# Optimization experiments

Hardware: AMD Instinct MI355X
Metric: run time of the kernel (lower is better)

Reference implementation:

```python
import jax, jax.numpy as jnp
import numpy as np

N_U = 50000   # num user nodes
N_I = 50000   # num item nodes
D = 64        # in_size == out_size
H = 128       # SemanticAttention hidden size (default)
E = 500000    # edges per meta-path graph
NEG_SLOPE = 0.01


def setup_inputs() -> dict:
    key = jax.random.key(0)
    ks = jax.random.split(key, 24)
    rn = lambda k, shp, s=0.1: jax.random.normal(k, shp, jnp.float32) * s
    ri = lambda k, shp, n: jax.random.randint(k, shp, 0, n, dtype=jnp.int32)
    return dict(
        feat_user=rn(ks[0], (N_U, D)), feat_item=rn(ks[1], (N_I, D)),
        attn_l=rn(ks[2], (4, D)), attn_r=rn(ks[3], (4, D)),
        W_gc=rn(ks[4], (4, D, D)), b_gc=jnp.zeros((4, D), jnp.float32),
        sa_rel_W1=rn(ks[5], (D, H)), sa_rel_b1=jnp.zeros((H,), jnp.float32), sa_rel_w2=rn(ks[6], (H,)),
        sa_u_W1=rn(ks[7], (D, H)), sa_u_b1=jnp.zeros((H,), jnp.float32), sa_u_w2=rn(ks[8], (H,)),
        sa_i_W1=rn(ks[9], (D, H)), sa_i_b1=jnp.zeros((H,), jnp.float32), sa_i_w2=rn(ks[10], (H,)),
        rel_u_src=ri(ks[11], (2, E), N_I), rel_u_dst=ri(ks[12], (2, E), N_U),
        rel_i_src=ri(ks[13], (2, E), N_U), rel_i_dst=ri(ks[14], (2, E), N_I),
        mp_u_src=ri(ks[15], (2, E), N_U), mp_u_dst=ri(ks[16], (2, E), N_U),
        mp_i_src=ri(ks[17], (2, E), N_I), mp_i_dst=ri(ks[18], (2, E), N_I),
    )


def _edge_softmax(e, dst, n_dst):
    # segment-wise (per destination node) softmax over irregular edges
    m = jax.ops.segment_max(e, dst, num_segments=n_dst)
    ex = jnp.exp(e - m[dst])
    s = jax.ops.segment_sum(ex, dst, num_segments=n_dst)
    return ex / s[dst]


def _heco_gat(src, dst, feat_src, feat_dst, al, ar, n_dst):
    # HeCoGATConv: el = sum(ft_src*attn_l), er = sum(ft_dst*attn_r)
    el = feat_src @ al  # (N_src,)
    er = feat_dst @ ar  # (N_dst,)
    e = jax.nn.leaky_relu(el[src] + er[dst], NEG_SLOPE)  # (E,)
    a = _edge_softmax(e, dst, n_dst)
    out = jax.ops.segment_sum(feat_src[src] * a[:, None], dst, num_segments=n_dst)
    return jax.nn.elu(out)


def _graph_conv(src, dst, feat, W, b, n):
    # DGL GraphConv with norm='both', activation=elu
    ones = jnp.ones(src.shape, jnp.float32)
    deg_out = jax.ops.segment_sum(ones, src, num_segments=n)
    deg_in = jax.ops.segment_sum(ones, dst, num_segments=n)
    no = jnp.where(deg_out > 0, deg_out, 1.0) ** -0.5
    ni = jnp.where(deg_in > 0, deg_in, 1.0) ** -0.5
    h = feat * no[:, None]
    agg = jax.ops.segment_sum(h[src], dst, num_segments=n)
    agg = agg * ni[:, None]
    return jax.nn.elu(agg @ W + b)


def _semantic_attention(z, W1, b1, w2):
    # z: (N, M, D) -> (N, D)
    w = (jnp.tanh(z @ W1 + b1) @ w2).mean(0)  # (M,)
    beta = jax.nn.softmax(w)
    return jnp.einsum('nmd,m->nd', z, beta)


def reference(feat_user, feat_item, attn_l, attn_r, W_gc, b_gc,
              sa_rel_W1, sa_rel_b1, sa_rel_w2,
              sa_u_W1, sa_u_b1, sa_u_w2,
              sa_i_W1, sa_i_b1, sa_i_w2,
              rel_u_src, rel_u_dst, rel_i_src, rel_i_dst,
              mp_u_src, mp_u_dst, mp_i_src, mp_i_dst):
    # --- RelationalAGG: HeCo GAT over schema-level relations ---
    zu = jnp.stack([
        _heco_gat(rel_u_src[0], rel_u_dst[0], feat_item, feat_user, attn_l[0], attn_r[0], N_U),
        _heco_gat(rel_u_src[1], rel_u_dst[1], feat_item, feat_user, attn_l[1], attn_r[1], N_U),
    ], axis=1)  # (N_U, 2, D)
    rel_u = _semantic_attention(zu, sa_rel_W1, sa_rel_b1, sa_rel_w2)
    zi = jnp.stack([
        _heco_gat(rel_i_src[0], rel_i_dst[0], feat_user, feat_item, attn_l[2], attn_r[2], N_I),
        _heco_gat(rel_i_src[1], rel_i_dst[1], feat_user, feat_item, attn_l[3], attn_r[3], N_I),
    ], axis=1)
    rel_i = _semantic_attention(zi, sa_rel_W1, sa_rel_b1, sa_rel_w2)
    # --- HAN layers: GraphConv over meta-path reachable graphs ---
    hu = jnp.stack([
        _graph_conv(mp_u_src[0], mp_u_dst[0], feat_user, W_gc[0], b_gc[0], N_U),
        _graph_conv(mp_u_src[1], mp_u_dst[1], feat_user, W_gc[1], b_gc[1], N_U),
    ], axis=1)
    han_u = _semantic_attention(hu, sa_u_W1, sa_u_b1, sa_u_w2)
    hi = jnp.stack([
        _graph_conv(mp_i_src[0], mp_i_dst[0], feat_item, W_gc[2], b_gc[2], N_I),
        _graph_conv(mp_i_src[1], mp_i_dst[1], feat_item, W_gc[3], b_gc[3], N_I),
    ], axis=1)
    han_i = _semantic_attention(hi, sa_i_W1, sa_i_b1, sa_i_w2)
    user_emb = rel_u + han_u
    item_emb = rel_i + han_i
    return jnp.concatenate([user_emb, item_emb], axis=0)  # (N_U + N_I, D)
```

## Files before the change

### kernel.cpp

```cpp
#include <hip/hip_runtime.h>
#include <math.h>

#define NU 50000
#define NI 50000
#define NN 50000
#define DD 64
#define HHID 128
#define EE 500000
#define NEG_SLOPE 0.01f
#define NBKT 196
#define CAP 3072
#define TILE 8192
#define TPG 62
#define P1T 512
#define NIMG 12
#define AGGB 1563
#define SEMB 512

typedef _Float16 half_t;
typedef _Float16 half8 __attribute__((ext_vector_type(8)));
typedef _Float16 half4 __attribute__((ext_vector_type(4)));
typedef float f32x4 __attribute__((ext_vector_type(4)));
union H4 { uint2 u; half_t h[4]; };
union H8 { uint4 u; half_t h[8]; };
union HS { half8 h; int i[4]; uint4 u; };
union HS4 { half4 h; int i[2]; uint2 u; };
union HC { unsigned short us; half_t h; };

struct Ptr4c { const float* p[4]; };
struct Ptr4m { float*       p[4]; };
struct EdgeArgs { const int* src[8]; const int* dst[8]; };
struct GatArgs { const half_t* fsrc[4]; half_t* zout[4]; };
struct GcArgs  { const half_t* feat[4]; half_t* hout[4]; };
struct WArgs   { const float* el[4]; const float* er[4]; const int* deg_src; };
struct SemArgs { const half_t* z[4]; const float* W1[4]; const float* b1[4]; const float* w2[4]; };
struct PrepArgs {
    const float* featI; const float* featU;
    Ptr4c vi; Ptr4c vu; Ptr4m oi; Ptr4m ou;
    half_t* FBI; half_t* FBU;
    const float* W_gc; half_t* W16;
};

__global__ __launch_bounds__(256) void prep_kernel(PrepArgs pa) {
    int b = blockIdx.x;
    int t = threadIdx.x;
    if (b == 6250) {
        int g = t >> 6;
        int lane = t & 63;
        int cl = lane & 15, quad = lane >> 4;
#pragma unroll
        for (int nt = 0; nt < 4; nt++) {
#pragma unroll
            for (int kh = 0; kh < 2; kh++) {
                H8 o;
#pragma unroll
                for (int j = 0; j < 8; j++) {
                    int k = kh * 32 + quad * 8 + j;
                    int n = nt * 16 + cl;
                    o.h[j] = (half_t)pa.W_gc[g * 4096 + k * 64 + n];
                }
                *(uint4*)(pa.W16 + ((g * 8 + nt * 2 + kh) * 64 + lane) * 8) = o.u;
            }
        }
        return;
    }
    const float* feat; Ptr4c vecs; Ptr4m outs; half_t* fb16; int bb;
    if (b < 3125) { feat = pa.featI; vecs = pa.vi; outs = pa.oi; fb16 = pa.FBI; bb = b; }
    else          { feat = pa.featU; vecs = pa.vu; outs = pa.ou; fb16 = pa.FBU; bb = b - 3125; }
    int w = bb * 4 + (t >> 6);
    int lane = t & 63;
    int sub = lane >> 4, r = lane & 15;
    int node = w * 4 + sub;
    float4 f = *(const float4*)(feat + node * DD + r * 4);
    H4 o16;
    o16.h[0] = (half_t)f.x; o16.h[1] = (half_t)f.y; o16.h[2] = (half_t)f.z; o16.h[3] = (half_t)f.w;
    *(uint2*)(fb16 + node * DD + r * 4) = o16.u;
#pragma unroll
    for (int j = 0; j < 4; j++) {
        float4 vv = *(const float4*)(vecs.p[j] + r * 4);
        float val = f.x * vv.x + f.y * vv.y + f.z * vv.z + f.w * vv.w;
        val += __shfl_down(val, 8);
        val += __shfl_down(val, 4);
        val += __shfl_down(val, 2);
        val += __shfl_down(val, 1);
        if (r == 0) outs.p[j][node] = val;
    }
}

__global__ __launch_bounds__(P1T) void part1_kernel(EdgeArgs a, int* __restrict__ ccnt,
                                                    int* __restrict__ coarse) {
    __shared__ int bc_cnt[256], bc_scan[256], bc_start[256], bc_cur[256], bc_gbase[256];
    __shared__ int stage[TILE];
    int t = threadIdx.x;
    int g = blockIdx.x / TPG;
    int tile = blockIdx.x % TPG;
    int e0 = tile * TILE;
    int tile_n = min(TILE, EE - e0);
    bool cnt_only = g >= 8;
    const int* gk = (cnt_only ? a.src[g - 4] : a.dst[g]) + e0;
    const int* gs = cnt_only ? gk : (a.src[g] + e0);
    if (t < 256) bc_cnt[t] = 0;
    __syncthreads();
    for (int pos = t * 4; pos < tile_n; pos += P1T * 4) {
        int4 k4 = *(const int4*)(gk + pos);
        atomicAdd(&bc_cnt[k4.x >> 8], 1);
        atomicAdd(&bc_cnt[k4.y >> 8], 1);
        atomicAdd(&bc_cnt[k4.z >> 8], 1);
        atomicAdd(&bc_cnt[k4.w >> 8], 1);
    }
    __syncthreads();
    if (t < 256) bc_scan[t] = bc_cnt[t];
    __syncthreads();
    for (int off = 1; off < 256; off <<= 1) {
        int v = (t < 256 && t >= off) ? bc_scan[t - off] : 0;
        __syncthreads();
        if (t < 256) bc_scan[t] += v;
        __syncthreads();
    }
    if (t < 256) {
        int st = bc_scan[t] - bc_cnt[t];
        bc_start[t] = st;
        bc_cur[t] = st;
        bc_gbase[t] = (t < NBKT && bc_cnt[t] > 0) ? atomicAdd(&ccnt[g * NBKT + t], bc_cnt[t]) : 0;
    }
    __syncthreads();
    for (int pos = t * 4; pos < tile_n; pos += P1T * 4) {
        int4 k4 = *(const int4*)(gk + pos);
        int4 s4;
        if (cnt_only) { s4 = make_int4(0, 0, 0, 0); }
        else          { s4 = *(const int4*)(gs + pos); }
        int b0 = k4.x >> 8, b1 = k4.y >> 8, b2 = k4.z >> 8, b3 = k4.w >> 8;
        int sl0 = atomicAdd(&bc_cur[b0], 1);
        int sl1 = atomicAdd(&bc_cur[b1], 1);
        int sl2 = atomicAdd(&bc_cur[b2], 1);
        int sl3 = atomicAdd(&bc_cur[b3], 1);
        stage[sl0] = s4.x | ((k4.x & 255) << 16) | (b0 << 24);
        stage[sl1] = s4.y | ((k4.y & 255) << 16) | (b1 << 24);
        stage[sl2] = s4.z | ((k4.z & 255) << 16) | (b2 << 24);
        stage[sl3] = s4.w | ((k4.w & 255) << 16) | (b3 << 24);
    }
    __syncthreads();
    for (int j = t; j < tile_n; j += P1T) {
        int p = stage[j];
        int b = (unsigned)p >> 24;
        int pos = bc_gbase[b] + (j - bc_start[b]);
        if (pos < CAP) coarse[(g * NBKT + b) * CAP + pos] = p & 0x00FFFFFF;
    }
}

__global__ __launch_bounds__(256) void degcnt_kernel(const int* __restrict__ ccnt,
                                                     const int* __restrict__ coarse,
                                                     int* __restrict__ DEG_SRC) {
    __shared__ int cnt[256];
    int t = threadIdx.x;
    int g2 = blockIdx.x / NBKT;
    int b = blockIdx.x % NBKT;
    int img = 8 + g2;
    int n = min(ccnt[img * NBKT + b], CAP);
    cnt[t] = 0;
    __syncthreads();
    const int* pairs = coarse + (img * NBKT + b) * CAP;
    for (int i = t; i < n; i += 256) atomicAdd(&cnt[(pairs[i] >> 16) & 255], 1);
    __syncthreads();
    int v = (b << 8) + t;
    if (v < NN) DEG_SRC[g2 * NN + v] = cnt[t];
}

__global__ __launch_bounds__(256) void part2_kernel(const int* __restrict__ ccnt,
                                                    const int* __restrict__ coarse,
                                                    WArgs wa,
                                                    int* __restrict__ bucket,
                                                    int2* __restrict__ RD) {
    __shared__ int sb[256];
    __shared__ int cnt5[256], off5[256], s2[256];
    __shared__ int ordered[CAP];
    int t = threadIdx.x;
    int g = blockIdx.x / NBKT;
    int b = blockIdx.x % NBKT;
    int ccv = (t < NBKT) ? min(ccnt[g * NBKT + t], CAP) : 0;
    sb[t] = ccv;
    cnt5[t] = 0;
    __syncthreads();
    for (int off = 1; off < 256; off <<= 1) {
        int vv = (t >= off) ? sb[t - off] : 0;
        __syncthreads();
        sb[t] += vv;
        __syncthreads();
    }
    int base = (b > 0) ? sb[b - 1] : 0;
    int n = sb[b] - base;
    int node0 = b << 8;
    const int* pairs = coarse + (g * NBKT + b) * CAP;
    for (int i = t; i < n; i += 256) atomicAdd(&cnt5[pairs[i] >> 16], 1);
    __syncthreads();
    int myc = cnt5[t];
    s2[t] = myc;
    __syncthreads();
    for (int off = 1; off < 256; off <<= 1) {
        int vv = (t >= off) ? s2[t - off] : 0;
        __syncthreads();
        s2[t] += vv;
        __syncthreads();
    }
    int ex = s2[t] - myc;
    off5[t] = ex;
    int v = node0 + t;
    if (v < NN) RD[g * NN + v] = make_int2(base + ex, myc);
    __syncthreads();
    int nm1 = n - 1;
    for (int ib = t; ib < n; ib += 1024) {
        int p[4];
#pragma unroll
        for (int u = 0; u < 4; u++) {
            int i = ib + u * 256;
            p[u] = pairs[(i < n) ? i : nm1];
        }
        float w[4];
        if (g < 4) {
            float a0[4], a1[4];
#pragma unroll
            for (int u = 0; u < 4; u++) a0[u] = wa.el[g][p[u] & 0xFFFF];
#pragma unroll
            for (int u = 0; u < 4; u++) a1[u] = wa.er[g][node0 + (p[u] >> 16)];
#pragma unroll
            for (int u = 0; u < 4; u++) {
                float e = a0[u] + a1[u];
                e = (e >= 0.f) ? e : NEG_SLOPE * e;
                w[u] = __expf(e);
            }
        } else {
            int dv[4];
#pragma unroll
            for (int u = 0; u < 4; u++) dv[u] = wa.deg_src[(g - 4) * NN + (p[u] & 0xFFFF)];
#pragma unroll
            for (int u = 0; u < 4; u++) w[u] = __builtin_amdgcn_rsqf((float)dv[u]);
        }
#pragma unroll
        for (int u = 0; u < 4; u++) {
            int i = ib + u * 256;
            if (i < n) {
                HC cv; cv.h = (half_t)w[u];
                int slot = atomicAdd(&off5[p[u] >> 16], 1);
                ordered[slot] = (p[u] & 0xFFFF) | ((int)cv.us << 16);
            }
        }
    }
    __syncthreads();
    int* bko = bucket + g * EE + base;
    for (int i = t; i < n; i += 256) bko[i] = ordered[i];
}

__global__ __launch_bounds__(256) void agg_kernel(GatArgs ga, GcArgs gc, half_t* __restrict__ AGG,
                                                  const int2* __restrict__ RD,
                                                  const int* __restrict__ bucket) {
    int h = blockIdx.x / (8 * AGGB);
    int remb = blockIdx.x % (8 * AGGB);
    int g = remb / AGGB;
    int nb = remb % AGGB;
    int t = threadIdx.x;
    int wv = t >> 6, lane = t & 63;
    int q = lane >> 3, r = lane & 7;
    int v = nb * 32 + wv * 8 + q;
    bool vok = v < NN;
    int2 rd = RD[g * NN + (vok ? v : 0)];
    int start = rd.x;
    int dg = vok ? rd.y : 0;
    const int* bk = bucket + g * EE;
    const half_t* feat = (g < 4) ? ga.fsrc[g] : gc.feat[g - 4];
    int roff = h * 32 + (r << 2);
    int obase = lane & 56;
    HS4 acc[4];
#pragma unroll
    for (int a = 0; a < 4; a++) { acc[a].i[0] = 0; acc[a].i[1] = 0; }
    float s_l = 0.f;
    for (int b8 = 0; b8 < dg; b8 += 8) {
        int rem = dg - b8;
        int p = bk[start + b8 + ((r < rem) ? r : 0)];
#pragma unroll
        for (int j = 0; j < 8; j++) {
            if (j < rem) {
                int pj = __shfl(p, obase + j);
                HC wj; wj.us = (unsigned short)((unsigned)pj >> 16);
                s_l += (float)wj.h;
                HS4 row; row.u = *(const uint2*)(feat + (((pj & 0xFFFF) << 6) + roff));
                half_t wh = wj.h;
                half4 ws = {wh, wh, wh, wh};
                acc[j & 3].h += row.h * ws;
            }
        }
    }
    acc[0].h += acc[1].h;
    acc[2].h += acc[3].h;
    acc[0].h += acc[2].h;
    if (g < 4) {
        float inv = (dg > 0) ? __builtin_amdgcn_rcpf(s_l) : 0.f;
        H4 o;
#pragma unroll
        for (int i = 0; i < 4; i++) {
            float x = (float)acc[0].h[i] * inv;
            x = (x > 0.f) ? x : (__expf(x) - 1.f);
            o.h[i] = (half_t)x;
        }
        if (vok) *(uint2*)(ga.zout[g] + (v << 7) + roff) = o.u;
    } else {
        float niv = (dg > 0) ? __builtin_amdgcn_rsqf((float)dg) : 1.0f;
        H4 o;
#pragma unroll
        for (int i = 0; i < 4; i++) o.h[i] = (half_t)((float)acc[0].h[i] * niv);
        if (vok) *(uint2*)(AGG + (((g - 4) * NN + v) << 6) + roff) = o.u;
    }
}

__global__ __launch_bounds__(256) void trans_kernel(GcArgs gc, const half_t* __restrict__ AGG,
                                                    const half_t* __restrict__ W16,
                                                    const float* __restrict__ b_gc) {
    int t = threadIdx.x;
    int wv = t >> 6, lane = t & 63;
    int g = blockIdx.x / 782;
    int tile = (blockIdx.x % 782) * 4 + wv;
    if (tile >= 3125) return;
    int cl = lane & 15, quad = lane >> 4;
    const half_t* ab = AGG + ((g * NN + tile * 16 + cl) << 6);
    half8 A0 = *(const half8*)(ab + quad * 8);
    half8 A1 = *(const half8*)(ab + 32 + quad * 8);
    const half_t* wbase = W16 + g * 8 * 64 * 8;
    half_t* hout = gc.hout[g];
#pragma unroll
    for (int nt = 0; nt < 4; nt++) {
        float bb = b_gc[g * 64 + nt * 16 + cl];
        f32x4 c = {bb, bb, bb, bb};
        half8 B0 = *(const half8*)(wbase + ((nt * 2 + 0) * 64 + lane) * 8);
        half8 B1 = *(const half8*)(wbase + ((nt * 2 + 1) * 64 + lane) * 8);
        c = __builtin_amdgcn_mfma_f32_16x16x32_f16(A0, B0, c, 0, 0, 0);
        c = __builtin_amdgcn_mfma_f32_16x16x32_f16(A1, B1, c, 0, 0, 0);
#pragma unroll
        for (int r_ = 0; r_ < 4; r_++) {
            int node = tile * 16 + quad * 4 + r_;
            float x = c[r_];
            x = (x > 0.f) ? x : (__expf(x) - 1.f);
            hout[node * 128 + nt * 16 + cl] = (half_t)x;
        }
    }
}

__global__ __launch_bounds__(256) void sem_att_kernel(SemArgs sa, float* __restrict__ wsum) {
    __shared__ half_t As[2][4][1024];
    __shared__ float s0[4], s1[4];
    int inst = blockIdx.x / SEMB;
    int blk  = blockIdx.x % SEMB;
    int t = threadIdx.x;
    int wv = t >> 6, lane = t & 63;
    int quad = lane >> 4, cl = lane & 15;
    const half_t* z = sa.z[inst];
    const float* W1 = sa.W1[inst];
    half8 Bf[2][2];
    float b1v[2], w2v[2];
#pragma unroll
    for (int u = 0; u < 2; u++) {
        int nt = wv * 2 + u;
        int n = nt * 16 + cl;
#pragma unroll
        for (int kh = 0; kh < 2; kh++) {
#pragma unroll
            for (int j = 0; j < 8; j++) {
                int k = kh * 32 + quad * 8 + j;
                Bf[u][kh][j] = (half_t)W1[k * HHID + n];
            }
        }
        b1v[u] = sa.b1[inst][nt * 16 + cl];
        w2v[u] = sa.w2[inst][nt * 16 + cl];
    }
    float local0 = 0.f, local1 = 0.f;
    int K = (6250 - blk + SEMB - 1) / SEMB;
    int B = (K + 3) / 4;

#define SEM_STAGE(buf, bb) { \
    int k_ = 4 * (bb) + wv; \
    if (k_ < K) { \
        int tp_ = blk + k_ * SEMB; \
        int m_ = (tp_ >= 3125) ? 1 : 0; \
        int tm_ = tp_ - m_ * 3125; \
        int n_ = lane >> 3; \
        int j_ = (lane & 7) * 8; \
        const half_t* sA_ = z + (size_t)(tm_ * 16 + n_) * 128 + m_ * 64 + j_; \
        const half_t* sB_ = z + (size_t)(tm_ * 16 + 8 + n_) * 128 + m_ * 64 + j_; \
        __builtin_amdgcn_global_load_lds( \
            (const __attribute__((address_space(1))) unsigned int*)sA_, \
            (__attribute__((address_space(3))) unsigned int*)(&As[buf][wv][0]), 16, 0, 0); \
        __builtin_amdgcn_global_load_lds( \
            (const __attribute__((address_space(1))) unsigned int*)sB_, \
            (__attribute__((address_space(3))) unsigned int*)(&As[buf][wv][512]), 16, 0, 0); \
    } }

    int cur = 0;
    SEM_STAGE(0, 0);
    for (int b = 0; b < B; b++) {
        if (b + 1 < B) {
            SEM_STAGE(cur ^ 1, b + 1);
            asm volatile("s_waitcnt vmcnt(2)" ::: "memory");
        } else {
            asm volatile("s_waitcnt vmcnt(0)" ::: "memory");
        }
        __builtin_amdgcn_sched_barrier(0);
        __builtin_amdgcn_s_barrier();
#pragma unroll
        for (int i = 0; i < 4; i++) {
            int k = 4 * b + i;
            if (k < K) {
                int tile = blk + k * SEMB;
                const half_t* ar = &As[cur][i][cl * 64 + quad * 8];
                half8 A0 = *(const half8*)(ar);
                half8 A1 = *(const half8*)(ar + 32);
                float sumv = 0.f;
#pragma unroll
                for (int u = 0; u < 2; u++) {
                    f32x4 c = {0.f, 0.f, 0.f, 0.f};
                    c = __builtin_amdgcn_mfma_f32_16x16x32_f16(A0, Bf[u][0], c, 0, 0, 0);
                    c = __builtin_amdgcn_mfma_f32_16x16x32_f16(A1, Bf[u][1], c, 0, 0, 0);
#pragma unroll
                    for (int r = 0; r < 4; r++) {
                        float xv = c[r] + b1v[u];
                        float ev = __expf(2.f * xv);
                        float th = 1.f - 2.f * __builtin_amdgcn_rcpf(ev + 1.f);
                        sumv += th * w2v[u];
                    }
                }
                if (tile < 3125) local0 += sumv; else local1 += sumv;
            }
        }
        __builtin_amdgcn_s_barrier();
        cur ^= 1;
    }
#undef SEM_STAGE
#pragma unroll
    for (int off = 32; off > 0; off >>= 1) {
        local0 += __shfl_down(local0, off);
        local1 += __shfl_down(local1, off);
    }
    if (lane == 0) { s0[wv] = local0; s1[wv] = local1; }
    __syncthreads();
    if (t == 0) {
        float a0 = s0[0] + s0[1] + s0[2] + s0[3];
        float a1 = s1[0] + s1[1] + s1[2] + s1[3];
        if (a0 != 0.f) atomicAdd(&wsum[inst * 2 + 0], a0);
        if (a1 != 0.f) atomicAdd(&wsum[inst * 2 + 1], a1);
    }
}

__global__ void combine_kernel(const half_t* __restrict__ ZU, const half_t* __restrict__ ZI,
                               const half_t* __restrict__ HU, const half_t* __restrict__ HI,
                               const float* __restrict__ wsum, float* __restrict__ out) {
    int gid = blockIdx.x * blockDim.x + threadIdx.x;
    if (gid >= (NU + NI) * 16) return;
    int node = gid >> 4;
    int c4 = (gid & 15) * 4;
    const half_t* zb; const half_t* hb;
    float wr0, wr1, wh0, wh1;
    int idx;
    if (node < NU) {
        zb = ZU; hb = HU; idx = node;
        wr0 = wsum[0]; wr1 = wsum[1]; wh0 = wsum[4]; wh1 = wsum[5];
    } else {
        zb = ZI; hb = HI; idx = node - NU;
        wr0 = wsum[2]; wr1 = wsum[3]; wh0 = wsum[6]; wh1 = wsum[7];
    }
    const float inv_n = 1.0f / 50000.0f;
    wr0 *= inv_n; wr1 *= inv_n; wh0 *= inv_n; wh1 *= inv_n;
    float m = fmaxf(wr0, wr1);
    float e0 = __expf(wr0 - m), e1 = __expf(wr1 - m);
    float br0 = e0 / (e0 + e1), br1 = e1 / (e0 + e1);
    m = fmaxf(wh0, wh1);
    e0 = __expf(wh0 - m); e1 = __expf(wh1 - m);
    float bh0 = e0 / (e0 + e1), bh1 = e1 / (e0 + e1);
    H4 z0, z1, h0, h1;
    z0.u = *(const uint2*)(zb + idx * 128 + c4);
    z1.u = *(const uint2*)(zb + idx * 128 + 64 + c4);
    h0.u = *(const uint2*)(hb + idx * 128 + c4);
    h1.u = *(const uint2*)(hb + idx * 128 + 64 + c4);
    float4 o;
    o.x = (float)z0.h[0] * br0 + (float)z1.h[0] * br1 + (float)h0.h[0] * bh0 + (float)h1.h[0] * bh1;
    o.y = (float)z0.h[1] * br0 + (float)z1.h[1] * br1 + (float)h0.h[1] * bh0 + (float)h1.h[1] * bh1;
    o.z = (float)z0.h[2] * br0 + (float)z1.h[2] * br1 + (float)h0.h[2] * bh0 + (float)h1.h[2] * bh1;
    o.w = (float)z0.h[3] * br0 + (float)z1.h[3] * br1 + (float)h0.h[3] * bh0 + (float)h1.h[3] * bh1;
    *(float4*)(out + node * 64 + c4) = o;
}

extern "C" void kernel_launch(void* const* d_in, const int* in_sizes, int n_in,
                              void* d_out, int out_size, void* d_ws, size_t ws_size,
                              hipStream_t stream) {
    const float* feat_user = (const float*)d_in[0];
    const float* feat_item = (const float*)d_in[1];
    const float* attn_l    = (const float*)d_in[2];
    const float* attn_r    = (const float*)d_in[3];
    const float* W_gc      = (const float*)d_in[4];
    const float* b_gc      = (const float*)d_in[5];
    const float* sa_rel_W1 = (const float*)d_in[6];
    const float* sa_rel_b1 = (const float*)d_in[7];
    const float* sa_rel_w2 = (const float*)d_in[8];
    const float* sa_u_W1   = (const float*)d_in[9];
    const float* sa_u_b1   = (const float*)d_in[10];
    const float* sa_u_w2   = (const float*)d_in[11];
    const float* sa_i_W1   = (const float*)d_in[12];
    const float* sa_i_b1   = (const float*)d_in[13];
    const float* sa_i_w2   = (const float*)d_in[14];
    const int* rel_u_src = (const int*)d_in[15];
    const int* rel_u_dst = (const int*)d_in[16];
    const int* rel_i_src = (const int*)d_in[17];
    const int* rel_i_dst = (const int*)d_in[18];
    const int* mp_u_src  = (const int*)d_in[19];
    const int* mp_u_dst  = (const int*)d_in[20];
    const int* mp_i_src  = (const int*)d_in[21];
    const int* mp_i_dst  = (const int*)d_in[22];

    half_t* ZU   = (half_t*)d_ws;
    half_t* ZI   = ZU + NN * 128;
    half_t* HU   = ZI + NN * 128;
    half_t* HI   = HU + NN * 128;
    half_t* FBU  = HI + NN * 128;
    half_t* FBI  = FBU + NN * 64;
    float*  DI   = (float*)(FBI + NN * 64);
    float*  DU   = DI + 4 * NN;
    int2*   RD   = (int2*)(DU + 4 * NN);
    int*    BUCKET = (int*)(RD + 8 * NN);
    int*    CCNT = BUCKET + 8 * EE;
    int*    DEG_SRC = CCNT + 12 * 256;
    float*  WSUM = (float*)(DEG_SRC + 4 * NN);
    half_t* W16  = (half_t*)(WSUM + 8);
    half_t* AGG  = W16 + 4 * 4096;
    int*    COARSE = (int*)d_ws;

    hipMemsetAsync(CCNT, 0, (size_t)(12 * 256 + 4 * NN) * sizeof(int) + 8 * sizeof(float), stream);

    PrepArgs pa;
    pa.featI = feat_item; pa.featU = feat_user;
    pa.vi = Ptr4c{{ attn_l + 0 * DD, attn_l + 1 * DD, attn_r + 2 * DD, attn_r + 3 * DD }};
    pa.oi = Ptr4m{{ DI, DI + NI, DI + 2 * NI, DI + 3 * NI }};
    pa.vu = Ptr4c{{ attn_l + 2 * DD, attn_l + 3 * DD, attn_r + 0 * DD, attn_r + 1 * DD }};
    pa.ou = Ptr4m{{ DU, DU + NU, DU + 2 * NU, DU + 3 * NU }};
    pa.FBI = FBI; pa.FBU = FBU;
    pa.W_gc = W_gc; pa.W16 = W16;
    prep_kernel<<<6251, 256, 0, stream>>>(pa);

    EdgeArgs ea;
    ea.src[0] = rel_u_src;      ea.dst[0] = rel_u_dst;
    ea.src[1] = rel_u_src + EE; ea.dst[1] = rel_u_dst + EE;
    ea.src[2] = rel_i_src;      ea.dst[2] = rel_i_dst;
    ea.src[3] = rel_i_src + EE; ea.dst[3] = rel_i_dst + EE;
    ea.src[4] = mp_u_src;       ea.dst[4] = mp_u_dst;
    ea.src[5] = mp_u_src + EE;  ea.dst[5] = mp_u_dst + EE;
    ea.src[6] = mp_i_src;       ea.dst[6] = mp_i_dst;
    ea.src[7] = mp_i_src + EE;  ea.dst[7] = mp_i_dst + EE;

    part1_kernel<<<NIMG * TPG, P1T, 0, stream>>>(ea, CCNT, COARSE);
    degcnt_kernel<<<4 * NBKT, 256, 0, stream>>>(CCNT, COARSE, DEG_SRC);

    WArgs wa;
    wa.el[0] = DI;      wa.er[0] = DU + 2 * NU;
    wa.el[1] = DI + NI; wa.er[1] = DU + 3 * NU;
    wa.el[2] = DU;      wa.er[2] = DI + 2 * NI;
    wa.el[3] = DU + NU; wa.er[3] = DI + 3 * NI;
    wa.deg_src = DEG_SRC;
    part2_kernel<<<8 * NBKT, 256, 0, stream>>>(CCNT, COARSE, wa, BUCKET, RD);

    GatArgs ga;
    ga.fsrc[0] = FBI; ga.zout[0] = ZU;
    ga.fsrc[1] = FBI; ga.zout[1] = ZU + 64;
    ga.fsrc[2] = FBU; ga.zout[2] = ZI;
    ga.fsrc[3] = FBU; ga.zout[3] = ZI + 64;
    GcArgs gc;
    gc.feat[0] = FBU; gc.hout[0] = HU;
    gc.feat[1] = FBU; gc.hout[1] = HU + 64;
    gc.feat[2] = FBI; gc.hout[2] = HI;
    gc.feat[3] = FBI; gc.hout[3] = HI + 64;
    agg_kernel<<<16 * AGGB, 256, 0, stream>>>(ga, gc, AGG, RD, BUCKET);

    trans_kernel<<<4 * 782, 256, 0, stream>>>(gc, AGG, W16, b_gc);

    SemArgs sa;
    sa.z[0] = ZU; sa.W1[0] = sa_rel_W1; sa.b1[0] = sa_rel_b1; sa.w2[0] = sa_rel_w2;
    sa.z[1] = ZI; sa.W1[1] = sa_rel_W1; sa.b1[1] = sa_rel_b1; sa.w2[1] = sa_rel_w2;
    sa.z[2] = HU; sa.W1[2] = sa_u_W1;   sa.b1[2] = sa_u_b1;   sa.w2[2] = sa_u_w2;
    sa.z[3] = HI; sa.W1[3] = sa_i_W1;   sa.b1[3] = sa_i_b1;   sa.w2[3] = sa_i_w2;
    sem_att_kernel<<<4 * SEMB, 256, 0, stream>>>(sa, WSUM);

    combine_kernel<<<((NU + NI) * 16 + 255) / 256, 256, 0, stream>>>(ZU, ZI, HU, HI, WSUM, (float*)d_out);
}
```

Before: 386.1 us.

## Fuse prep into edge-bucketing kernel and widen aggregation to full rows

```diff
diff --git a/kernel.cpp b/kernel.cpp
--- a/kernel.cpp
+++ b/kernel.cpp
@@ -14,17 +14,16 @@
 #define TPG 62
 #define P1T 512
 #define NIMG 12
+#define P1B (NIMG * TPG)
 #define AGGB 1563
 #define SEMB 512
 
 typedef _Float16 half_t;
 typedef _Float16 half8 __attribute__((ext_vector_type(8)));
-typedef _Float16 half4 __attribute__((ext_vector_type(4)));
 typedef float f32x4 __attribute__((ext_vector_type(4)));
 union H4 { uint2 u; half_t h[4]; };
 union H8 { uint4 u; half_t h[8]; };
 union HS { half8 h; int i[4]; uint4 u; };
-union HS4 { half4 h; int i[2]; uint2 u; };
 union HC { unsigned short us; half_t h; };
 
 struct Ptr4c { const float* p[4]; };
@@ -41,57 +40,60 @@
     const float* W_gc; half_t* W16;
 };
 
-__global__ __launch_bounds__(256) void prep_kernel(PrepArgs pa) {
-    int b = blockIdx.x;
-    int t = threadIdx.x;
-    if (b == 6250) {
-        int g = t >> 6;
-        int lane = t & 63;
-        int cl = lane & 15, quad = lane >> 4;
-#pragma unroll
-        for (int nt = 0; nt < 4; nt++) {
-#pragma unroll
-            for (int kh = 0; kh < 2; kh++) {
-                H8 o;
-#pragma unroll
-                for (int j = 0; j < 8; j++) {
-                    int k = kh * 32 + quad * 8 + j;
-                    int n = nt * 16 + cl;
-                    o.h[j] = (half_t)pa.W_gc[g * 4096 + k * 64 + n];
-                }
-                *(uint4*)(pa.W16 + ((g * 8 + nt * 2 + kh) * 64 + lane) * 8) = o.u;
-            }
-        }
-        return;
-    }
-    const float* feat; Ptr4c vecs; Ptr4m outs; half_t* fb16; int bb;
-    if (b < 3125) { feat = pa.featI; vecs = pa.vi; outs = pa.oi; fb16 = pa.FBI; bb = b; }
-    else          { feat = pa.featU; vecs = pa.vu; outs = pa.ou; fb16 = pa.FBU; bb = b - 3125; }
-    int w = bb * 4 + (t >> 6);
-    int lane = t & 63;
-    int sub = lane >> 4, r = lane & 15;
-    int node = w * 4 + sub;
-    float4 f = *(const float4*)(feat + node * DD + r * 4);
-    H4 o16;
-    o16.h[0] = (half_t)f.x; o16.h[1] = (half_t)f.y; o16.h[2] = (half_t)f.z; o16.h[3] = (half_t)f.w;
-    *(uint2*)(fb16 + node * DD + r * 4) = o16.u;
-#pragma unroll
-    for (int j = 0; j < 4; j++) {
-        float4 vv = *(const float4*)(vecs.p[j] + r * 4);
-        float val = f.x * vv.x + f.y * vv.y + f.z * vv.z + f.w * vv.w;
-        val += __shfl_down(val, 8);
-        val += __shfl_down(val, 4);
-        val += __shfl_down(val, 2);
-        val += __shfl_down(val, 1);
-        if (r == 0) outs.p[j][node] = val;
-    }
-}
-
-__global__ __launch_bounds__(P1T) void part1_kernel(EdgeArgs a, int* __restrict__ ccnt,
-                                                    int* __restrict__ coarse) {
+__global__ __launch_bounds__(P1T) void build_kernel(EdgeArgs a, int* __restrict__ ccnt,
+                                                    int* __restrict__ coarse, PrepArgs pa) {
     __shared__ int bc_cnt[256], bc_scan[256], bc_start[256], bc_cur[256], bc_gbase[256];
     __shared__ int stage[TILE];
     int t = threadIdx.x;
+    if (blockIdx.x >= P1B) {
+        int pb = blockIdx.x - P1B;
+        if (pb == 3125) {
+            if (t < 256) {
+                int g = t >> 6;
+                int lane = t & 63;
+                int cl = lane & 15, quad = lane >> 4;
+#pragma unroll
+                for (int nt = 0; nt < 4; nt++) {
+#pragma unroll
+                    for (int kh = 0; kh < 2; kh++) {
+                        H8 o;
+#pragma unroll
+                        for (int j = 0; j < 8; j++) {
+                            int k = kh * 32 + quad * 8 + j;
+                            int n = nt * 16 + cl;
+                            o.h[j] = (half_t)pa.W_gc[g * 4096 + k * 64 + n];
+                        }
+                        *(uint4*)(pa.W16 + ((g * 8 + nt * 2 + kh) * 64 + lane) * 8) = o.u;
+                    }
+                }
+            }
+            return;
+        }
+        int ob = pb * 2 + (t >> 8);
+        int t256 = t & 255;
+        const float* feat; Ptr4c vecs; Ptr4m outs; half_t* fb16; int bb;
+        if (ob < 3125) { feat = pa.featI; vecs = pa.vi; outs = pa.oi; fb16 = pa.FBI; bb = ob; }
+        else           { feat = pa.featU; vecs = pa.vu; outs = pa.ou; fb16 = pa.FBU; bb = ob - 3125; }
+        int w = bb * 4 + (t256 >> 6);
+        int lane = t256 & 63;
+        int sub = lane >> 4, r = lane & 15;
+        int node = w * 4 + sub;
+        float4 f = *(const float4*)(feat + node * DD + r * 4);
+        H4 o16;
+        o16.h[0] = (half_t)f.x; o16.h[1] = (half_t)f.y; o16.h[2] = (half_t)f.z; o16.h[3] = (half_t)f.w;
+        *(uint2*)(fb16 + node * DD + r * 4) = o16.u;
+#pragma unroll
+        for (int j = 0; j < 4; j++) {
+            float4 vv = *(const float4*)(vecs.p[j] + r * 4);
+            float val = f.x * vv.x + f.y * vv.y + f.z * vv.z + f.w * vv.w;
+            val += __shfl_down(val, 8);
+            val += __shfl_down(val, 4);
+            val += __shfl_down(val, 2);
+            val += __shfl_down(val, 1);
+            if (r == 0) outs.p[j][node] = val;
+        }
+        return;
+    }
     int g = blockIdx.x / TPG;
     int tile = blockIdx.x % TPG;
     int e0 = tile * TILE;
@@ -253,10 +255,8 @@
 __global__ __launch_bounds__(256) void agg_kernel(GatArgs ga, GcArgs gc, half_t* __restrict__ AGG,
                                                   const int2* __restrict__ RD,
                                                   const int* __restrict__ bucket) {
-    int h = blockIdx.x / (8 * AGGB);
-    int remb = blockIdx.x % (8 * AGGB);
-    int g = remb / AGGB;
-    int nb = remb % AGGB;
+    int g = blockIdx.x / AGGB;
+    int nb = blockIdx.x % AGGB;
     int t = threadIdx.x;
     int wv = t >> 6, lane = t & 63;
     int q = lane >> 3, r = lane & 7;
@@ -267,11 +267,13 @@
     int dg = vok ? rd.y : 0;
     const int* bk = bucket + g * EE;
     const half_t* feat = (g < 4) ? ga.fsrc[g] : gc.feat[g - 4];
-    int roff = h * 32 + (r << 2);
+    int roff = r << 3;
     int obase = lane & 56;
-    HS4 acc[4];
-#pragma unroll
-    for (int a = 0; a < 4; a++) { acc[a].i[0] = 0; acc[a].i[1] = 0; }
+    HS acc[4];
+#pragma unroll
+    for (int a = 0; a < 4; a++)
+#pragma unroll
+        for (int j = 0; j < 4; j++) acc[a].i[j] = 0;
     float s_l = 0.f;
     for (int b8 = 0; b8 < dg; b8 += 8) {
         int rem = dg - b8;
@@ -282,9 +284,9 @@
                 int pj = __shfl(p, obase + j);
                 HC wj; wj.us = (unsigned short)((unsigned)pj >> 16);
                 s_l += (float)wj.h;
-                HS4 row; row.u = *(const uint2*)(feat + (((pj & 0xFFFF) << 6) + roff));
+                HS row; row.u = *(const uint4*)(feat + (((pj & 0xFFFF) << 6) + roff));
                 half_t wh = wj.h;
-                half4 ws = {wh, wh, wh, wh};
+                half8 ws = {wh, wh, wh, wh, wh, wh, wh, wh};
                 acc[j & 3].h += row.h * ws;
             }
         }
@@ -294,20 +296,20 @@
     acc[0].h += acc[2].h;
     if (g < 4) {
         float inv = (dg > 0) ? __builtin_amdgcn_rcpf(s_l) : 0.f;
-        H4 o;
-#pragma unroll
-        for (int i = 0; i < 4; i++) {
+        H8 o;
+#pragma unroll
+        for (int i = 0; i < 8; i++) {
             float x = (float)acc[0].h[i] * inv;
             x = (x > 0.f) ? x : (__expf(x) - 1.f);
             o.h[i] = (half_t)x;
         }
-        if (vok) *(uint2*)(ga.zout[g] + (v << 7) + roff) = o.u;
+        if (vok) *(uint4*)(ga.zout[g] + (v << 7) + roff) = o.u;
     } else {
         float niv = (dg > 0) ? __builtin_amdgcn_rsqf((float)dg) : 1.0f;
-        H4 o;
-#pragma unroll
-        for (int i = 0; i < 4; i++) o.h[i] = (half_t)((float)acc[0].h[i] * niv);
-        if (vok) *(uint2*)(AGG + (((g - 4) * NN + v) << 6) + roff) = o.u;
+        H8 o;
+#pragma unroll
+        for (int i = 0; i < 8; i++) o.h[i] = (half_t)((float)acc[0].h[i] * niv);
+        if (vok) *(uint4*)(AGG + (((g - 4) * NN + v) << 6) + roff) = o.u;
     }
 }
 
@@ -539,7 +541,6 @@
     pa.ou = Ptr4m{{ DU, DU + NU, DU + 2 * NU, DU + 3 * NU }};
     pa.FBI = FBI; pa.FBU = FBU;
     pa.W_gc = W_gc; pa.W16 = W16;
-    prep_kernel<<<6251, 256, 0, stream>>>(pa);
 
     EdgeArgs ea;
     ea.src[0] = rel_u_src;      ea.dst[0] = rel_u_dst;
@@ -551,7 +552,7 @@
     ea.src[6] = mp_i_src;       ea.dst[6] = mp_i_dst;
     ea.src[7] = mp_i_src + EE;  ea.dst[7] = mp_i_dst + EE;
 
-    part1_kernel<<<NIMG * TPG, P1T, 0, stream>>>(ea, CCNT, COARSE);
+    build_kernel<<<P1B + 3126, P1T, 0, stream>>>(ea, CCNT, COARSE, pa);
     degcnt_kernel<<<4 * NBKT, 256, 0, stream>>>(CCNT, COARSE, DEG_SRC);
 
     WArgs wa;
@@ -572,7 +573,7 @@
     gc.feat[1] = FBU; gc.hout[1] = HU + 64;
     gc.feat[2] = FBI; gc.hout[2] = HI;
     gc.feat[3] = FBI; gc.hout[3] = HI + 64;
-    agg_kernel<<<16 * AGGB, 256, 0, stream>>>(ga, gc, AGG, RD, BUCKET);
+    agg_kernel<<<8 * AGGB, 256, 0, stream>>>(ga, gc, AGG, RD, BUCKET);
 
     trans_kernel<<<4 * 782, 256, 0, stream>>>(gc, AGG, W16, b_gc);
 
```

Measured after the change: 329.6 us. 14.6% less time.
